# Optimization experiments

Hardware: AMD Instinct MI355X
Metric: run time of the kernel (lower is better)

The kernel has to match this reference:

```python
import jax, jax.numpy as jnp
import numpy as np

H, DM, DK, DV = 16, 1024, 64, 64
S, B = 2048, 2


def setup_inputs() -> dict:
    key = jax.random.key(0)
    ks = jax.random.split(key, 7)
    u = 1.0 / np.sqrt(DM)
    uo = 1.0 / np.sqrt(H * DV)
    return {
        "Q": jax.random.normal(ks[0], (S, B, DM), jnp.float32),
        "K": jax.random.normal(ks[1], (S, B, DM), jnp.float32),
        "V": jax.random.normal(ks[2], (S, B, DM), jnp.float32),
        "WQ": jax.random.uniform(ks[3], (H, DM, DK), jnp.float32, -u, u),
        "WK": jax.random.uniform(ks[4], (H, DM, DK), jnp.float32, -u, u),
        "WV": jax.random.uniform(ks[5], (H, DM, DV), jnp.float32, -u, u),
        "WO": jax.random.uniform(ks[6], (H * DV, DM), jnp.float32, -uo, uo),
    }


def reference(Q, K, V, WQ, WK, WV, WO):
    # Layout: (seq, batch, feat); heads stacked as leading dim of weights.
    q = jnp.einsum('sbm,hmk->hsbk', Q, WQ)   # [H,S,B,DK]
    k = jnp.einsum('sbm,hmk->hsbk', K, WK)
    v = jnp.einsum('sbm,hmv->hsbv', V, WV)
    scores = jnp.einsum('hsbk,htbk->hsbt', q, k) / jnp.sqrt(jnp.asarray(DK, q.dtype))
    # Causal mask: key index t > query index s gets -inf (matches triu inf subtract).
    causal = jnp.arange(S)[None, :] > jnp.arange(S)[:, None]  # [S_q, S_k]
    scores = jnp.where(causal[None, :, None, :], -jnp.inf, scores)
    p = jax.nn.softmax(scores, axis=-1)
    o = jnp.einsum('hsbt,htbv->hsbv', p, v)  # [H,S,B,DV]
    y = jnp.transpose(o, (1, 2, 0, 3)).reshape(S, B, H * DV)  # concat heads on dim 2
    return y @ WO  # [S,B,DM]
```

## Files before the change

### kernel.cpp

```cpp
#include <hip/hip_runtime.h>
#include <hip/hip_bf16.h>


typedef __bf16 bf16;
typedef bf16 bf16x8 __attribute__((ext_vector_type(8)));
typedef bf16 bf16x4 __attribute__((ext_vector_type(4)));
typedef float f32x4 __attribute__((ext_vector_type(4)));

#define MFMA16(a, b, c) __builtin_amdgcn_mfma_f32_16x16x32_bf16((a), (b), (c), 0, 0, 0)

static __device__ __forceinline__ bf16x8 load8(const bf16* p) {
  return *reinterpret_cast<const bf16x8*>(p);
}
static __device__ __forceinline__ void store8(bf16* p, bf16x8 v) {
  *reinterpret_cast<bf16x8*>(p) = v;
}
static __device__ __forceinline__ void store4(bf16* p, bf16x4 v) {
  *reinterpret_cast<bf16x4*>(p) = v;
}
static __device__ __forceinline__ bf16x8 cvt8(float4 a, float4 b) {
  bf16x8 o;
  o[0] = (bf16)a.x; o[1] = (bf16)a.y; o[2] = (bf16)a.z; o[3] = (bf16)a.w;
  o[4] = (bf16)b.x; o[5] = (bf16)b.y; o[6] = (bf16)b.z; o[7] = (bf16)b.w;
  return o;
}
static __device__ __forceinline__ f32x4 zero4() {
  f32x4 v; v[0] = 0.f; v[1] = 0.f; v[2] = 0.f; v[3] = 0.f; return v;
}
static __device__ __forceinline__ void gload_lds16(const void* g, void* l) {
  __builtin_amdgcn_global_load_lds(
      (const __attribute__((address_space(1))) void*)g,
      (__attribute__((address_space(3))) void*)l, 16, 0, 0);
}

__global__ __launch_bounds__(256) void wcvt_kernel(const float* __restrict__ WQ,
                                                   const float* __restrict__ WK,
                                                   const float* __restrict__ WV,
                                                   bf16* __restrict__ out) {
  __shared__ float tile[32][33];
  const int zz = blockIdx.z;
  const int tau = zz >> 4;
  const float* in = ((tau == 0) ? WQ : (tau == 1) ? WK : WV) + (size_t)(zz & 15) * 65536;
  bf16* o = out + (size_t)zz * 65536;
  const float scale = (tau == 0) ? 0.125f * 1.44269504f : 1.0f;
  const int r0 = blockIdx.y * 32, c0 = blockIdx.x * 32;
  const int tx = threadIdx.x & 31, ty = threadIdx.x >> 5;
#pragma unroll
  for (int i = 0; i < 32; i += 8) tile[ty + i][tx] = in[(size_t)(r0 + ty + i) * 64 + c0 + tx];
  __syncthreads();
#pragma unroll
  for (int i = 0; i < 32; i += 8)
    o[(size_t)(c0 + ty + i) * 1024 + r0 + tx] = (bf16)(tile[tx][ty + i] * scale);
}

__global__ __launch_bounds__(256) void tcvt_kernel(const float* __restrict__ in,
                                                   bf16* __restrict__ out, int R, int C) {
  __shared__ float tile[32][33];
  const int r0 = blockIdx.y * 32, c0 = blockIdx.x * 32;
  const int tx = threadIdx.x & 31, ty = threadIdx.x >> 5;
#pragma unroll
  for (int i = 0; i < 32; i += 8) tile[ty + i][tx] = in[(size_t)(r0 + ty + i) * C + c0 + tx];
  __syncthreads();
#pragma unroll
  for (int i = 0; i < 32; i += 8)
    out[(size_t)(c0 + ty + i) * R + r0 + tx] = (bf16)tile[tx][ty + i];
}

__global__ __launch_bounds__(256) void proj_kernel(
    const float* __restrict__ X0, const float* __restrict__ X1, const float* __restrict__ X2,
    const bf16* __restrict__ Wt, bf16* __restrict__ qws, bf16* __restrict__ kws,
    bf16* __restrict__ vtws) {
  const int id = blockIdx.x;
  const int n = id / 96;
  const int w = id % 96;
  const int z = w >> 5;
  const int m = w & 31;
  const float* X = (z == 0) ? X0 : ((z == 1) ? X1 : X2);
  const bf16* Wz = Wt + (size_t)z * 1024 * 1024;
  const int mBase = m * 128;
  const int nBase = n * 128;

  __shared__ float Afl[2][128 * 32];
  __shared__ bf16 Bl[2][128 * 32];

  const int t = threadIdx.x;
  const int lane = t & 63;
  const int wave = t >> 6;
  const int wm = (wave >> 1) * 64;
  const int wn = (wave & 1) * 64;
  const int ln = lane & 15;
  const int quad = lane >> 4;
  const int bswz = quad ^ ((ln >> 1) & 3);

  f32x4 acc[4][4];
#pragma unroll
  for (int i = 0; i < 4; i++)
#pragma unroll
    for (int j = 0; j < 4; j++) acc[i][j] = zero4();

  auto issueA = [&](int k0, float* dst) {
#pragma unroll
    for (int i = 0; i < 4; i++) {
      const int c = i * 256 + t;
      const int mp = c >> 3;
      const int ql = (c & 7) ^ (mp & 7);
      gload_lds16(X + (size_t)(mBase + mp) * 1024 + k0 + ql * 4,
                  dst + (i * 256 + wave * 64) * 4);
    }
  };
  auto issueB = [&](int k0, bf16* dst) {
#pragma unroll
    for (int i = 0; i < 2; i++) {
      const int c = i * 256 + t;
      const int mp = c >> 2;
      const int ql = (c & 3) ^ ((mp >> 1) & 3);
      gload_lds16(Wz + (size_t)(nBase + mp) * 1024 + k0 + ql * 8,
                  dst + (i * 256 + wave * 64) * 8);
    }
  };

  issueB(0, Bl[0]);
  issueA(0, Afl[0]);
  __syncthreads();

  for (int k0 = 0; k0 < 1024; k0 += 32) {
    const int cur = (k0 >> 5) & 1, nxt = cur ^ 1;
    const bool more = (k0 + 32) < 1024;
    if (more) {
      issueB(k0 + 32, Bl[nxt]);
      issueA(k0 + 32, Afl[nxt]);
    }
    bf16x8 a[4], bfr[4];
#pragma unroll
    for (int i = 0; i < 4; i++) {
      const int mrow = wm + i * 16 + ln;
      const float4 f0 = *reinterpret_cast<const float4*>(
          &Afl[cur][(mrow * 8 + ((2 * quad) ^ (mrow & 7))) * 4]);
      const float4 f1 = *reinterpret_cast<const float4*>(
          &Afl[cur][(mrow * 8 + ((2 * quad + 1) ^ (mrow & 7))) * 4]);
      a[i] = cvt8(f0, f1);
    }
#pragma unroll
    for (int j = 0; j < 4; j++) bfr[j] = load8(&Bl[cur][((wn + j * 16 + ln) * 4 + bswz) * 8]);
#pragma unroll
    for (int i = 0; i < 4; i++)
#pragma unroll
      for (int j = 0; j < 4; j++) acc[i][j] = MFMA16(a[i], bfr[j], acc[i][j]);
    __syncthreads();
  }

#pragma unroll
  for (int i = 0; i < 4; i++) {
#pragma unroll
    for (int j = 0; j < 4; j++) {
      const int col = nBase + wn + j * 16 + ln;
      const int h = col >> 6, d = col & 63;
#pragma unroll
      for (int r = 0; r < 4; r++) {
        const int row = mBase + wm + i * 16 + quad * 4 + r;
        const int s = row >> 1, bb = row & 1;
        const int hb = h * 2 + bb;
        const bf16 val = (bf16)acc[i][j][r];
        if (z == 0) {
          qws[((size_t)hb * 2048 + s) * 64 + d] = val;
        } else if (z == 1) {
          kws[((size_t)hb * 2048 + s) * 64 + d] = val;
        } else {
          const int pos = (s & ~63) | ((s & 15) << 2) | ((s >> 4) & 3);
          vtws[((size_t)hb * 64 + d) * 2048 + pos] = val;
        }
      }
    }
  }
}

__global__ __launch_bounds__(256, 3) void attn_kernel(
    const bf16* __restrict__ qws, const bf16* __restrict__ kws, const bf16* __restrict__ vtws,
    bf16* __restrict__ cc) {
  const int id = blockIdx.x;
  const int hb = id & 31;
  const int qb = 15 - (id >> 5);
  const int q0 = qb * 128;
  const int h = hb >> 1, b = hb & 1;

  const int t = threadIdx.x;
  const int lane = t & 63;
  const int wave = t >> 6;
  const int ln = lane & 15;
  const int quad = lane >> 4;
  const int swz3 = ln & 7;

  const bf16* qh = qws + (size_t)hb * 2048 * 64;
  const bf16* kh = kws + (size_t)hb * 2048 * 64;
  const bf16* vh = vtws + (size_t)hb * 64 * 2048;

  __shared__ bf16 Kl[2][64 * 64];
  __shared__ bf16 Pl[4][32 * 72];
  bf16* Plw = &Pl[wave][0];

  bf16x8 ones;
#pragma unroll
  for (int i = 0; i < 8; i++) ones[i] = (bf16)1.0f;

  bf16x8 qf[2][2];
#pragma unroll
  for (int mb = 0; mb < 2; mb++)
#pragma unroll
    for (int hh = 0; hh < 2; hh++)
      qf[mb][hh] = load8(qh + (size_t)(q0 + wave * 32 + mb * 16 + ln) * 64 + hh * 32 + quad * 8);

  f32x4 accO[2][4];
  f32x4 accL[2];
#pragma unroll
  for (int mb = 0; mb < 2; mb++) {
    accL[mb] = zero4();
#pragma unroll
    for (int d = 0; d < 4; d++) accO[mb][d] = zero4();
  }

#pragma unroll
  for (int i = 0; i < 2; i++) {
    const int c = i * 256 + t;
    const int mp = c >> 3;
    const int ql = (c & 7) ^ (mp & 7);
    gload_lds16(kh + (size_t)mp * 64 + ql * 8, &Kl[0][(i * 256 + wave * 64) * 8]);
  }

  const int Jmax = 2 * qb + 2;
  for (int jt = 0; jt < Jmax; jt++) {
    const int kt0 = jt * 64;
    const int cur = jt & 1, nxt = cur ^ 1;
    __syncthreads();
    if (jt + 1 < Jmax) {
      const int nt0 = kt0 + 64;
#pragma unroll
      for (int i = 0; i < 2; i++) {
        const int c = i * 256 + t;
        const int mp = c >> 3;
        const int ql = (c & 7) ^ (mp & 7);
        gload_lds16(kh + (size_t)(nt0 + mp) * 64 + ql * 8, &Kl[nxt][(i * 256 + wave * 64) * 8]);
      }
    }

    f32x4 sv[2][4];
#pragma unroll
    for (int nt = 0; nt < 4; nt++) {
      const int mm = nt * 16 + ln;
      bf16x8 b0 = load8(&Kl[cur][(mm * 8 + (quad ^ swz3)) * 8]);
      bf16x8 b1 = load8(&Kl[cur][(mm * 8 + ((quad + 4) ^ swz3)) * 8]);
#pragma unroll
      for (int mb = 0; mb < 2; mb++) {
        f32x4 s = MFMA16(qf[mb][0], b0, zero4());
        s = MFMA16(qf[mb][1], b1, s);
        sv[mb][nt] = s;
      }
    }

    bf16x8 vb[2][4];
#pragma unroll
    for (int ks = 0; ks < 2; ks++)
#pragma unroll
      for (int d = 0; d < 4; d++)
        vb[ks][d] = load8(vh + (size_t)(d * 16 + ln) * 2048 + kt0 + (ks * 4 + quad) * 8);

    if (jt >= 2 * qb) {
#pragma unroll
      for (int mb = 0; mb < 2; mb++)
#pragma unroll
        for (int nt = 0; nt < 4; nt++) {
          const int kg = kt0 + nt * 16 + ln;
#pragma unroll
          for (int r = 0; r < 4; r++) {
            const int qg = q0 + wave * 32 + mb * 16 + quad * 4 + r;
            if (kg > qg) sv[mb][nt][r] = -1e30f;
          }
        }
    }

#pragma unroll
    for (int mb = 0; mb < 2; mb++) {
#pragma unroll
      for (int r = 0; r < 4; r++) {
        const int row = mb * 16 + quad * 4 + r;
        bf16x4 pw;
#pragma unroll
        for (int nt = 0; nt < 4; nt++) pw[nt] = (bf16)exp2f(sv[mb][nt][r]);
        store4(Plw + row * 72 + ln * 4, pw);
      }
    }

#pragma unroll
    for (int ks = 0; ks < 2; ks++) {
      bf16x8 pa[2];
#pragma unroll
      for (int mb = 0; mb < 2; mb++)
        pa[mb] = load8(Plw + (mb * 16 + ln) * 72 + (ks * 4 + quad) * 8);
#pragma unroll
      for (int d = 0; d < 4; d++)
#pragma unroll
        for (int mb = 0; mb < 2; mb++) accO[mb][d] = MFMA16(pa[mb], vb[ks][d], accO[mb][d]);
#pragma unroll
      for (int mb = 0; mb < 2; mb++) accL[mb] = MFMA16(pa[mb], ones, accL[mb]);
    }
  }

#pragma unroll
  for (int mb = 0; mb < 2; mb++) {
#pragma unroll
    for (int r = 0; r < 4; r++) {
      const float inv = 1.0f / accL[mb][r];
      const int s = q0 + wave * 32 + mb * 16 + quad * 4 + r;
#pragma unroll
      for (int d = 0; d < 4; d++)
        cc[((size_t)s * 2 + b) * 1024 + h * 64 + d * 16 + ln] = (bf16)(accO[mb][d][r] * inv);
    }
  }
}

__global__ __launch_bounds__(256) void out_kernel(
    const bf16* __restrict__ A, const bf16* __restrict__ Bt, float* __restrict__ outp) {
  const int id = blockIdx.x;
  const int nb = id >> 6;
  const int mb = id & 63;
  const int mBase = mb * 64, nBase = nb * 128;

  __shared__ bf16 Al[2][64 * 32];
  __shared__ bf16 Bl[2][128 * 32];

  const int t = threadIdx.x;
  const int lane = t & 63;
  const int wave = t >> 6;
  const int wm = (wave >> 1) * 32;
  const int wn = (wave & 1) * 64;
  const int ln = lane & 15;
  const int quad = lane >> 4;
  const int bswz = quad ^ ((ln >> 1) & 3);

  f32x4 acc[2][4];
#pragma unroll
  for (int i = 0; i < 2; i++)
#pragma unroll
    for (int j = 0; j < 4; j++) acc[i][j] = zero4();

  const int amp = t >> 2, aql = (t & 3) ^ ((amp >> 1) & 3);

  gload_lds16(A + (size_t)(mBase + amp) * 1024 + aql * 8, &Al[0][(wave * 64) * 8]);
#pragma unroll
  for (int i = 0; i < 2; i++) {
    const int c = i * 256 + t;
    const int mp = c >> 2, ql = (c & 3) ^ ((mp >> 1) & 3);
    gload_lds16(Bt + (size_t)(nBase + mp) * 1024 + ql * 8, &Bl[0][(i * 256 + wave * 64) * 8]);
  }
  __syncthreads();

  for (int k0 = 0; k0 < 1024; k0 += 32) {
    const int cur = (k0 >> 5) & 1, nxt = cur ^ 1;
    const bool more = (k0 + 32) < 1024;
    if (more) {
      gload_lds16(A + (size_t)(mBase + amp) * 1024 + k0 + 32 + aql * 8, &Al[nxt][(wave * 64) * 8]);
#pragma unroll
      for (int i = 0; i < 2; i++) {
        const int c = i * 256 + t;
        const int mp = c >> 2, ql = (c & 3) ^ ((mp >> 1) & 3);
        gload_lds16(Bt + (size_t)(nBase + mp) * 1024 + k0 + 32 + ql * 8,
                    &Bl[nxt][(i * 256 + wave * 64) * 8]);
      }
    }
    bf16x8 a[2], bfr[4];
#pragma unroll
    for (int i = 0; i < 2; i++) a[i] = load8(&Al[cur][((wm + i * 16 + ln) * 4 + bswz) * 8]);
#pragma unroll
    for (int jj = 0; jj < 4; jj++) bfr[jj] = load8(&Bl[cur][((wn + jj * 16 + ln) * 4 + bswz) * 8]);
#pragma unroll
    for (int i = 0; i < 2; i++)
#pragma unroll
      for (int jj = 0; jj < 4; jj++) acc[i][jj] = MFMA16(a[i], bfr[jj], acc[i][jj]);
    __syncthreads();
  }

#pragma unroll
  for (int i = 0; i < 2; i++)
#pragma unroll
    for (int jj = 0; jj < 4; jj++)
#pragma unroll
      for (int r = 0; r < 4; r++)
        outp[(size_t)(mBase + wm + i * 16 + quad * 4 + r) * 1024 + nBase + wn + jj * 16 + ln] =
            acc[i][jj][r];
}

extern "C" void kernel_launch(void* const* d_in, const int* in_sizes, int n_in,
                              void* d_out, int out_size, void* d_ws, size_t ws_size,
                              hipStream_t stream) {
  (void)in_sizes; (void)n_in; (void)out_size; (void)ws_size;
  const float* Q  = (const float*)d_in[0];
  const float* K  = (const float*)d_in[1];
  const float* V  = (const float*)d_in[2];
  const float* WQ = (const float*)d_in[3];
  const float* WK = (const float*)d_in[4];
  const float* WV = (const float*)d_in[5];
  const float* WO = (const float*)d_in[6];
  float* outp = (float*)d_out;

  const size_t REG = (size_t)4 * 1024 * 1024;
  bf16* base = (bf16*)d_ws;
  bf16* Wt   = base;
  bf16* cc   = base;
  bf16* qws  = base + REG;
  bf16* WOt  = base + REG;
  bf16* kws  = base + 2 * REG;
  bf16* vtws = base + 3 * REG;

  wcvt_kernel<<<dim3(2, 32, 48), 256, 0, stream>>>(WQ, WK, WV, Wt);
  proj_kernel<<<dim3(768), 256, 0, stream>>>(Q, K, V, Wt, qws, kws, vtws);
  attn_kernel<<<dim3(512), 256, 0, stream>>>(qws, kws, vtws, cc);
  tcvt_kernel<<<dim3(32, 32, 1), 256, 0, stream>>>(WO, WOt, 1024, 1024);
  out_kernel<<<dim3(8 * 64), 256, 0, stream>>>(cc, WOt, outp);
}
```

Baseline: 235.4 us.

## Retile attention to 64-row query blocks with 128-key tiles and swizzled P

Attention blocks now cover 64 queries (16 per wave) instead of 128, doubling grid size to 1024, while key tiles grow from 64 to 128 keys per iteration. The V transpose permutation in the projection kernel is changed to match 128-key groups, and the P staging buffer uses an XOR swizzle instead of padding. The intent is to increase parallelism and cut per-iteration overhead (syncs, masking only on the last tile). The tradeoff is less K/V reuse per block: each loaded K tile serves half as many queries, and causal masking now wastes up to half of the final 128-key tile.

```diff
diff --git a/kernel.cpp b/kernel.cpp
--- a/kernel.cpp
+++ b/kernel.cpp
@@ -14,9 +14,6 @@
 }
 static __device__ __forceinline__ void store8(bf16* p, bf16x8 v) {
   *reinterpret_cast<bf16x8*>(p) = v;
-}
-static __device__ __forceinline__ void store4(bf16* p, bf16x4 v) {
-  *reinterpret_cast<bf16x4*>(p) = v;
 }
 static __device__ __forceinline__ bf16x8 cvt8(float4 a, float4 b) {
   bf16x8 o;
@@ -166,7 +163,7 @@
         } else if (z == 1) {
           kws[((size_t)hb * 2048 + s) * 64 + d] = val;
         } else {
-          const int pos = (s & ~63) | ((s & 15) << 2) | ((s >> 4) & 3);
+          const int pos = (s & ~127) | ((s & 15) << 3) | ((s >> 4) & 7);
           vtws[((size_t)hb * 64 + d) * 2048 + pos] = val;
         }
       }
@@ -179,8 +176,8 @@
     bf16* __restrict__ cc) {
   const int id = blockIdx.x;
   const int hb = id & 31;
-  const int qb = 15 - (id >> 5);
-  const int q0 = qb * 128;
+  const int qq = 31 - (id >> 5);
+  const int q0 = qq * 64;
   const int h = hb >> 1, b = hb & 1;
 
   const int t = threadIdx.x;
@@ -194,47 +191,41 @@
   const bf16* kh = kws + (size_t)hb * 2048 * 64;
   const bf16* vh = vtws + (size_t)hb * 64 * 2048;
 
-  __shared__ bf16 Kl[2][64 * 64];
-  __shared__ bf16 Pl[4][32 * 72];
+  __shared__ bf16 Kl[2][128 * 64];
+  __shared__ bf16 Pl[4][16 * 128];
   bf16* Plw = &Pl[wave][0];
 
   bf16x8 ones;
 #pragma unroll
   for (int i = 0; i < 8; i++) ones[i] = (bf16)1.0f;
 
-  bf16x8 qf[2][2];
-#pragma unroll
-  for (int mb = 0; mb < 2; mb++)
-#pragma unroll
-    for (int hh = 0; hh < 2; hh++)
-      qf[mb][hh] = load8(qh + (size_t)(q0 + wave * 32 + mb * 16 + ln) * 64 + hh * 32 + quad * 8);
-
-  f32x4 accO[2][4];
-  f32x4 accL[2];
-#pragma unroll
-  for (int mb = 0; mb < 2; mb++) {
-    accL[mb] = zero4();
-#pragma unroll
-    for (int d = 0; d < 4; d++) accO[mb][d] = zero4();
-  }
-
-#pragma unroll
-  for (int i = 0; i < 2; i++) {
+  bf16x8 qf[2];
+#pragma unroll
+  for (int hh = 0; hh < 2; hh++)
+    qf[hh] = load8(qh + (size_t)(q0 + wave * 16 + ln) * 64 + hh * 32 + quad * 8);
+
+  f32x4 accO[4];
+  f32x4 accL = zero4();
+#pragma unroll
+  for (int d = 0; d < 4; d++) accO[d] = zero4();
+
+#pragma unroll
+  for (int i = 0; i < 4; i++) {
     const int c = i * 256 + t;
     const int mp = c >> 3;
     const int ql = (c & 7) ^ (mp & 7);
     gload_lds16(kh + (size_t)mp * 64 + ql * 8, &Kl[0][(i * 256 + wave * 64) * 8]);
   }
 
-  const int Jmax = 2 * qb + 2;
+  const int Jmax = (qq >> 1) + 1;
   for (int jt = 0; jt < Jmax; jt++) {
-    const int kt0 = jt * 64;
+    const int kt0 = jt * 128;
     const int cur = jt & 1, nxt = cur ^ 1;
     __syncthreads();
     if (jt + 1 < Jmax) {
-      const int nt0 = kt0 + 64;
-#pragma unroll
-      for (int i = 0; i < 2; i++) {
+      const int nt0 = kt0 + 128;
+#pragma unroll
+      for (int i = 0; i < 4; i++) {
         const int c = i * 256 + t;
         const int mp = c >> 3;
         const int ql = (c & 7) ^ (mp & 7);
@@ -242,78 +233,56 @@
       }
     }
 
-    f32x4 sv[2][4];
-#pragma unroll
-    for (int nt = 0; nt < 4; nt++) {
+    f32x4 sv[8];
+#pragma unroll
+    for (int nt = 0; nt < 8; nt++) {
       const int mm = nt * 16 + ln;
       bf16x8 b0 = load8(&Kl[cur][(mm * 8 + (quad ^ swz3)) * 8]);
       bf16x8 b1 = load8(&Kl[cur][(mm * 8 + ((quad + 4) ^ swz3)) * 8]);
-#pragma unroll
-      for (int mb = 0; mb < 2; mb++) {
-        f32x4 s = MFMA16(qf[mb][0], b0, zero4());
-        s = MFMA16(qf[mb][1], b1, s);
-        sv[mb][nt] = s;
-      }
-    }
-
-    bf16x8 vb[2][4];
-#pragma unroll
-    for (int ks = 0; ks < 2; ks++)
-#pragma unroll
-      for (int d = 0; d < 4; d++)
-        vb[ks][d] = load8(vh + (size_t)(d * 16 + ln) * 2048 + kt0 + (ks * 4 + quad) * 8);
-
-    if (jt >= 2 * qb) {
-#pragma unroll
-      for (int mb = 0; mb < 2; mb++)
-#pragma unroll
-        for (int nt = 0; nt < 4; nt++) {
-          const int kg = kt0 + nt * 16 + ln;
-#pragma unroll
-          for (int r = 0; r < 4; r++) {
-            const int qg = q0 + wave * 32 + mb * 16 + quad * 4 + r;
-            if (kg > qg) sv[mb][nt][r] = -1e30f;
-          }
+      f32x4 s = MFMA16(qf[0], b0, zero4());
+      sv[nt] = MFMA16(qf[1], b1, s);
+    }
+
+    if (jt == Jmax - 1) {
+#pragma unroll
+      for (int nt = 0; nt < 8; nt++) {
+        const int kg = kt0 + nt * 16 + ln;
+#pragma unroll
+        for (int r = 0; r < 4; r++) {
+          const int qg = q0 + wave * 16 + quad * 4 + r;
+          if (kg > qg) sv[nt][r] = -1e30f;
         }
-    }
-
-#pragma unroll
-    for (int mb = 0; mb < 2; mb++) {
-#pragma unroll
-      for (int r = 0; r < 4; r++) {
-        const int row = mb * 16 + quad * 4 + r;
-        bf16x4 pw;
-#pragma unroll
-        for (int nt = 0; nt < 4; nt++) pw[nt] = (bf16)exp2f(sv[mb][nt][r]);
-        store4(Plw + row * 72 + ln * 4, pw);
-      }
-    }
-
-#pragma unroll
-    for (int ks = 0; ks < 2; ks++) {
-      bf16x8 pa[2];
-#pragma unroll
-      for (int mb = 0; mb < 2; mb++)
-        pa[mb] = load8(Plw + (mb * 16 + ln) * 72 + (ks * 4 + quad) * 8);
-#pragma unroll
-      for (int d = 0; d < 4; d++)
-#pragma unroll
-        for (int mb = 0; mb < 2; mb++) accO[mb][d] = MFMA16(pa[mb], vb[ks][d], accO[mb][d]);
-#pragma unroll
-      for (int mb = 0; mb < 2; mb++) accL[mb] = MFMA16(pa[mb], ones, accL[mb]);
-    }
-  }
-
-#pragma unroll
-  for (int mb = 0; mb < 2; mb++) {
+      }
+    }
+
 #pragma unroll
     for (int r = 0; r < 4; r++) {
-      const float inv = 1.0f / accL[mb][r];
-      const int s = q0 + wave * 32 + mb * 16 + quad * 4 + r;
-#pragma unroll
-      for (int d = 0; d < 4; d++)
-        cc[((size_t)s * 2 + b) * 1024 + h * 64 + d * 16 + ln] = (bf16)(accO[mb][d][r] * inv);
-    }
+      const int row = quad * 4 + r;
+      bf16x8 pw;
+#pragma unroll
+      for (int nt = 0; nt < 8; nt++) pw[nt] = (bf16)exp2f(sv[nt][r]);
+      store8(Plw + (size_t)(row * 16 + (ln ^ (row & 7))) * 8, pw);
+    }
+
+#pragma unroll
+    for (int ks = 0; ks < 4; ks++) {
+      bf16x8 pa = load8(Plw + (size_t)(ln * 16 + ((ks * 4 + quad) ^ swz3)) * 8);
+#pragma unroll
+      for (int d = 0; d < 4; d++) {
+        bf16x8 vb = load8(vh + (size_t)(d * 16 + ln) * 2048 + kt0 + (ks * 4 + quad) * 8);
+        accO[d] = MFMA16(pa, vb, accO[d]);
+      }
+      accL = MFMA16(pa, ones, accL);
+    }
+  }
+
+#pragma unroll
+  for (int r = 0; r < 4; r++) {
+    const float inv = 1.0f / accL[r];
+    const int s = q0 + wave * 16 + quad * 4 + r;
+#pragma unroll
+    for (int d = 0; d < 4; d++)
+      cc[((size_t)s * 2 + b) * 1024 + h * 64 + d * 16 + ln] = (bf16)(accO[d][r] * inv);
   }
 }
 
@@ -412,7 +381,7 @@
 
   wcvt_kernel<<<dim3(2, 32, 48), 256, 0, stream>>>(WQ, WK, WV, Wt);
   proj_kernel<<<dim3(768), 256, 0, stream>>>(Q, K, V, Wt, qws, kws, vtws);
-  attn_kernel<<<dim3(512), 256, 0, stream>>>(qws, kws, vtws, cc);
+  attn_kernel<<<dim3(1024), 256, 0, stream>>>(qws, kws, vtws, cc);
   tcvt_kernel<<<dim3(32, 32, 1), 256, 0, stream>>>(WO, WOt, 1024, 1024);
   out_kernel<<<dim3(8 * 64), 256, 0, stream>>>(cc, WOt, outp);
 }
```

After: 258.1 us. 9.7% more time.
